# Kernel optimization log

Measured on AMD Instinct MI355X. Metric: run time of the kernel, lower is better.

The kernel has to match this reference:

```python
import jax, jax.numpy as jnp
import numpy as np

N_HEAD = 12
LN_EPS = 1e-5


def _layernorm(x, g, b):
    m = jnp.mean(x, axis=-1, keepdims=True)
    v = jnp.mean(jnp.square(x - m), axis=-1, keepdims=True)
    return (x - m) * jax.lax.rsqrt(v + LN_EPS) * g + b


def _block(x, p):
    # p holds single-layer params. x: [B, S, D]
    B, S, D = x.shape
    Dh = D // N_HEAD
    h = _layernorm(x, p['ln1_g'], p['ln1_b'])
    q = (h @ p['wq'] + p['bq']).reshape(B, S, N_HEAD, Dh)
    k = (h @ p['wk'] + p['bk']).reshape(B, S, N_HEAD, Dh)
    v = (h @ p['wv'] + p['bv']).reshape(B, S, N_HEAD, Dh)
    scores = jnp.einsum('bqhd,bkhd->bhqk', q, k) / np.sqrt(Dh).astype(x.dtype)
    causal = jnp.tril(jnp.ones((S, S), dtype=bool))  # valid_nums = arange(1..S)
    scores = jnp.where(causal, scores, -jnp.inf)
    attn = jax.nn.softmax(scores, axis=-1)  # dropout is identity in eval
    o = jnp.einsum('bhqk,bkhd->bqhd', attn, v).reshape(B, S, D)
    x = x + o @ p['wo'] + p['bo']
    h2 = _layernorm(x, p['ln2_g'], p['ln2_b'])
    ff = jax.nn.gelu(h2 @ p['w1'] + p['b1'], approximate=False) @ p['w2'] + p['b2']
    return x + ff


def _gpt_forward(idx, wte, wpe, layer_params, lnf_g, lnf_b, lm_w):
    S = idx.shape[1]
    x = wte[idx] + wpe[None, :S, :]  # embd dropout is identity in eval
    x = jax.lax.scan(lambda c, p: (_block(c, p), None), x, layer_params)[0]
    x = _layernorm(x, lnf_g, lnf_b)
    return x @ lm_w  # logits [B, S, V]


def setup_inputs() -> dict:
    B, S, D, V, L, F = 4, 1024, 768, 50257, 12, 3072
    key = jax.random.key(0)
    ks = iter(jax.random.split(key, 24))
    std = 0.02
    std_proj = 0.02 / np.sqrt(2 * L)  # special init for w_o / FFN.linear2

    def w(shape, s=std):
        return jax.random.normal(next(ks), shape, jnp.float32) * s

    return dict(
        idx=jax.random.randint(next(ks), (B, S), 0, V),
        wte=w((V, D)), wpe=w((S, D)),
        ln1_g=jnp.ones((L, D)), ln1_b=jnp.zeros((L, D)),
        wq=w((L, D, D)), bq=jnp.zeros((L, D)),
        wk=w((L, D, D)), bk=jnp.zeros((L, D)),
        wv=w((L, D, D)), bv=jnp.zeros((L, D)),
        wo=w((L, D, D), std_proj), bo=jnp.zeros((L, D)),
        ln2_g=jnp.ones((L, D)), ln2_b=jnp.zeros((L, D)),
        w1=w((L, D, F)), b1=jnp.zeros((L, F)),
        w2=w((L, F, D), std_proj), b2=jnp.zeros((L, D)),
        lnf_g=jnp.ones((D,)), lnf_b=jnp.zeros((D,)),
        lm_w=w((D, V)),
    )


def reference(idx, wte, wpe, ln1_g, ln1_b, wq, bq, wk, bk, wv, bv, wo, bo,
              ln2_g, ln2_b, w1, b1, w2, b2, lnf_g, lnf_b, lm_w):
    layer_params = dict(ln1_g=ln1_g, ln1_b=ln1_b, wq=wq, bq=bq, wk=wk, bk=bk,
                        wv=wv, bv=bv, wo=wo, bo=bo, ln2_g=ln2_g, ln2_b=ln2_b,
                        w1=w1, b1=b1, w2=w2, b2=b2)
    return _gpt_forward(idx, wte, wpe, layer_params, lnf_g, lnf_b, lm_w)
```

## Files before the change

kernel.cpp:

```cpp
#include <hip/hip_runtime.h>
#include <hip/hip_bf16.h>

typedef __attribute__((ext_vector_type(8))) short short8;
typedef __attribute__((ext_vector_type(4))) short short4v;
typedef __attribute__((ext_vector_type(4))) float floatx4;

#define GLD16(g, l) __builtin_amdgcn_global_load_lds( \
    (__attribute__((address_space(1))) void*)(g),      \
    (__attribute__((address_space(3))) void*)(l), 16, 0, 0)

#define MFMA_BF16(a, b, c) __builtin_amdgcn_mfma_f32_16x16x32_bf16((a), (b), (c), 0, 0, 0)

__device__ __forceinline__ short f2bf(float f) {
  union { __hip_bfloat16 h; short s; } u;
  u.h = __float2bfloat16(f);
  return u.s;
}

template <int N>
__device__ __forceinline__ void wait_vm() {
  if constexpr (N == 0) asm volatile("s_waitcnt vmcnt(0)" ::: "memory");
  else if constexpr (N == 4) asm volatile("s_waitcnt vmcnt(4)" ::: "memory");
  else if constexpr (N == 6) asm volatile("s_waitcnt vmcnt(6)" ::: "memory");
}
__device__ __forceinline__ void cfence() { asm volatile("" ::: "memory"); }

__global__ __launch_bounds__(256)
void transpose_convert(const float* __restrict__ in, short* __restrict__ out,
                       const int K, const int N, const size_t inStride,
                       const size_t outStride) {
  in += blockIdx.z * inStride;
  out += blockIdx.z * outStride;
  __shared__ float tile[32][33];
  const int n0 = blockIdx.x * 32;
  const int k0 = blockIdx.y * 32;
  const int tx = threadIdx.x;
  const int ty = threadIdx.y;
#pragma unroll
  for (int i = 0; i < 4; ++i) {
    const int kk = ty + i * 8;
    const int nn = n0 + tx;
    tile[kk][tx] = (nn < N) ? in[(size_t)(k0 + kk) * N + nn] : 0.f;
  }
  __syncthreads();
#pragma unroll
  for (int i = 0; i < 4; ++i) {
    const int nn = ty + i * 8;
    out[(size_t)(n0 + nn) * K + k0 + tx] = f2bf(tile[tx][nn]);
  }
}

__global__ __launch_bounds__(256)
void embed_kernel(const int* __restrict__ idx, const float* __restrict__ wte,
                  const float* __restrict__ wpe, float* __restrict__ x) {
  const int row = blockIdx.x;
  const int tok = idx[row];
  const int s = row & 1023;
  const float* wt = wte + (size_t)tok * 768;
  const float* wp = wpe + (size_t)s * 768;
  float* xr = x + (size_t)row * 768;
  for (int c = threadIdx.x; c < 768; c += 256) xr[c] = wt[c] + wp[c];
}

__global__ __launch_bounds__(256)
void ln_kernel(const float* __restrict__ x, const float* __restrict__ g,
               const float* __restrict__ b, short* __restrict__ out) {
  const int wv = threadIdx.x >> 6, lane = threadIdx.x & 63;
  const int row = blockIdx.x * 4 + wv;
  const float* xr = x + (size_t)row * 768 + lane * 12;
  const float4 a0 = *(const float4*)(xr);
  const float4 a1 = *(const float4*)(xr + 4);
  const float4 a2 = *(const float4*)(xr + 8);
  float v[12] = {a0.x, a0.y, a0.z, a0.w, a1.x, a1.y, a1.z, a1.w,
                 a2.x, a2.y, a2.z, a2.w};
  float s = 0.f;
#pragma unroll
  for (int i = 0; i < 12; ++i) s += v[i];
#pragma unroll
  for (int m = 1; m < 64; m <<= 1) s += __shfl_xor(s, m);
  const float mean = s * (1.0f / 768.0f);
  float q = 0.f;
#pragma unroll
  for (int i = 0; i < 12; ++i) {
    v[i] -= mean;
    q += v[i] * v[i];
  }
#pragma unroll
  for (int m = 1; m < 64; m <<= 1) q += __shfl_xor(q, m);
  const float inv = rsqrtf(q * (1.0f / 768.0f) + 1e-5f);

  const float* gp = g + lane * 12;
  const float* bp = b + lane * 12;
  const float4 g0 = *(const float4*)(gp);
  const float4 g1 = *(const float4*)(gp + 4);
  const float4 g2 = *(const float4*)(gp + 8);
  const float4 b0 = *(const float4*)(bp);
  const float4 b1 = *(const float4*)(bp + 4);
  const float4 b2 = *(const float4*)(bp + 8);
  const float gg[12] = {g0.x, g0.y, g0.z, g0.w, g1.x, g1.y, g1.z, g1.w,
                        g2.x, g2.y, g2.z, g2.w};
  const float bb[12] = {b0.x, b0.y, b0.z, b0.w, b1.x, b1.y, b1.z, b1.w,
                        b2.x, b2.y, b2.z, b2.w};
  short r[12];
#pragma unroll
  for (int i = 0; i < 12; ++i) r[i] = f2bf(v[i] * inv * gg[i] + bb[i]);
  short* orow = out + (size_t)row * 768 + lane * 12;
#pragma unroll
  for (int i = 0; i < 3; ++i)
    *(short4v*)(orow + i * 4) = short4v{r[i * 4], r[i * 4 + 1], r[i * 4 + 2],
                                        r[i * 4 + 3]};
}

enum { EPI_QKV = 0, EPI_RESID = 1, EPI_GELU = 2 };

template <int BM, int BN, int EPI>
__global__ __launch_bounds__(256)
void gemm_kernel(const short* __restrict__ A, const short* __restrict__ Bt,
                 const int K,
                 const float* __restrict__ bias0, const float* __restrict__ bias1,
                 const float* __restrict__ bias2, float* __restrict__ fout,
                 short* __restrict__ bout0, short* __restrict__ bout1,
                 short* __restrict__ bout2) {
  constexpr int MF = BM / 32;
  constexpr int NF = BN / 32;
  constexpr int NL = MF + NF;
  __shared__ short sA[2][BM * 64];
  __shared__ short sB[2][BN * 64];
  const int tid = threadIdx.x;
  const int wv = tid >> 6;
  const int lane = tid & 63;
  const int lrow = lane & 15;
  const int lk8 = lane >> 4;
  const int m0 = blockIdx.x * BM;
  const int n0 = blockIdx.y * BN;
  const int wm = (wv >> 1) * (BM / 2);
  const int wn = (wv & 1) * (BN / 2);
  constexpr int MW = BM / 2 / 16;
  constexpr int NW = BN / 2 / 16;

  floatx4 acc[MW][NW];
#pragma unroll
  for (int m = 0; m < MW; ++m)
#pragma unroll
    for (int n = 0; n < NW; ++n) acc[m][n] = {0.f, 0.f, 0.f, 0.f};

  const short* pA[MF];
  const short* pB[NF];
#pragma unroll
  for (int i = 0; i < MF; ++i) {
    const int p = i * 256 + tid;
    const int rr = p >> 3, up = p & 7;
    pA[i] = A + (size_t)(m0 + rr) * K + ((up ^ (rr & 7)) << 3);
  }
#pragma unroll
  for (int i = 0; i < NF; ++i) {
    const int p = i * 256 + tid;
    const int rr = p >> 3, up = p & 7;
    pB[i] = Bt + (size_t)(n0 + rr) * K + ((up ^ (rr & 7)) << 3);
  }

  auto stage = [&](int buf) {
#pragma unroll
    for (int i = 0; i < MF; ++i) {
      GLD16(pA[i], sA[buf] + (i * 256 + wv * 64) * 8);
      pA[i] += 64;
    }
#pragma unroll
    for (int i = 0; i < NF; ++i) {
      GLD16(pB[i], sB[buf] + (i * 256 + wv * 64) * 8);
      pB[i] += 64;
    }
  };

  auto compute = [&](const short* pa, const short* pb) {
    const int xr = lrow & 7;
    short8 af[MW][2], bv[NW][2];
#pragma unroll
    for (int m = 0; m < MW; ++m) {
      const int row = (wm + m * 16 + lrow) * 64;
      af[m][0] = *(const short8*)(pa + row + ((lk8 ^ xr) << 3));
      af[m][1] = *(const short8*)(pa + row + (((4 + lk8) ^ xr) << 3));
    }
#pragma unroll
    for (int n = 0; n < NW; ++n) {
      const int row = (wn + n * 16 + lrow) * 64;
      bv[n][0] = *(const short8*)(pb + row + ((lk8 ^ xr) << 3));
      bv[n][1] = *(const short8*)(pb + row + (((4 + lk8) ^ xr) << 3));
    }
#pragma unroll
    for (int m = 0; m < MW; ++m)
#pragma unroll
      for (int n = 0; n < NW; ++n) {
        acc[m][n] = MFMA_BF16(af[m][0], bv[n][0], acc[m][n]);
        acc[m][n] = MFMA_BF16(af[m][1], bv[n][1], acc[m][n]);
      }
  };

  const int nk = K >> 6;
  stage(0);
  int cur = 0;
  for (int kt = 0; kt < nk; ++kt) {
    if (kt + 1 < nk) {
      stage(cur ^ 1);
      wait_vm<NL>();
    } else {
      wait_vm<0>();
    }
    __builtin_amdgcn_s_barrier();
    cfence();
    __builtin_amdgcn_s_setprio(1);
    compute(sA[cur], sB[cur]);
    __builtin_amdgcn_s_setprio(0);
    cfence();
    __builtin_amdgcn_s_barrier();
    cur ^= 1;
  }

#pragma unroll
  for (int m = 0; m < MW; ++m) {
#pragma unroll
    for (int n = 0; n < NW; ++n) {
#pragma unroll
      for (int r = 0; r < 4; ++r) {
        const float v = acc[m][n][r];
        const int gm = m0 + wm + m * 16 + lk8 * 4 + r;
        const int gn = n0 + wn + n * 16 + lrow;
        if (EPI == EPI_QKV) {
          const int sec = (gn >= 1536) ? 2 : (gn >= 768 ? 1 : 0);
          const int nn = gn - sec * 768;
          const int hh = nn >> 6, dh = nn & 63;
          const int bb = gm >> 10, srow = gm & 1023;
          if (sec == 0) {
            bout0[(((size_t)(bb * 12 + hh) * 1024 + srow) << 6) + dh] =
                f2bf((v + bias0[nn]) * 0.18033688f);
          } else if (sec == 1) {
            bout1[(((size_t)(bb * 12 + hh) * 1024 + srow) << 6) + dh] =
                f2bf(v + bias1[nn]);
          } else {
            bout2[(((size_t)(bb * 12 + hh) * 64 + dh) << 10) + srow] =
                f2bf(v + bias2[nn]);
          }
        } else if (EPI == EPI_RESID) {
          float* xp = fout + (size_t)gm * 768 + gn;
          *xp = *xp + v + bias0[gn];
        } else {
          const float tt = v + bias0[gn];
          const float gl = 0.5f * tt * (1.f + erff(tt * 0.70710678118654752f));
          bout0[(size_t)gm * 3072 + gn] = f2bf(gl);
        }
      }
    }
  }
}

__global__ __launch_bounds__(512, 2)
void gemm_lm_kernel(const short* __restrict__ A, const short* __restrict__ Bt,
                    float* __restrict__ fout) {
  __shared__ short sA[2][256 * 64];
  __shared__ short sB[2][128 * 64];
  const int K = 768;
  const int tid = threadIdx.x;
  const int wv = tid >> 6;
  const int lane = tid & 63;
  const int lrow = lane & 15;
  const int lk8 = lane >> 4;
  const int m0 = blockIdx.x * 256;
  const int n0 = blockIdx.y * 128;
  const int wm = (wv >> 1) * 64;
  const int wn = (wv & 1) * 64;

  floatx4 acc[4][4];
#pragma unroll
  for (int m = 0; m < 4; ++m)
#pragma unroll
    for (int n = 0; n < 4; ++n) acc[m][n] = {0.f, 0.f, 0.f, 0.f};

  const short* Ab = A + (size_t)m0 * K;
  const short* Bb = Bt + (size_t)n0 * K;

  const short* pA[4];
  const short* pB[2];
#pragma unroll
  for (int i = 0; i < 4; ++i) {
    const int p = i * 512 + tid;
    const int rr = p >> 3, up = p & 7;
    pA[i] = Ab + (size_t)rr * K + ((up ^ (rr & 7)) << 3);
  }
#pragma unroll
  for (int i = 0; i < 2; ++i) {
    const int p = i * 512 + tid;
    const int rr = p >> 3, up = p & 7;
    pB[i] = Bb + (size_t)rr * K + ((up ^ (rr & 7)) << 3);
  }

  auto stage = [&](int buf) {
#pragma unroll
    for (int i = 0; i < 4; ++i) {
      GLD16(pA[i], sA[buf] + (i * 512 + wv * 64) * 8);
      pA[i] += 64;
    }
#pragma unroll
    for (int i = 0; i < 2; ++i) {
      GLD16(pB[i], sB[buf] + (i * 512 + wv * 64) * 8);
      pB[i] += 64;
    }
  };

  const int arow = (wm + lrow) * 64;
  const int xr = (lrow & 7);

  stage(0);
  int cur = 0;
  for (int kt = 0; kt < 12; ++kt) {
    if (kt + 1 < 12) {
      stage(cur ^ 1);
      wait_vm<6>();
    } else {
      wait_vm<0>();
    }
    __builtin_amdgcn_s_barrier();
    cfence();

    const short* pa = sA[cur];
    const short* pb = sB[cur];
    short8 bvv[4][2];
#pragma unroll
    for (int n = 0; n < 4; ++n) {
      const int brow = (wn + n * 16 + lrow) * 64;
      bvv[n][0] = *(const short8*)(pb + brow + ((lk8 ^ xr) << 3));
      bvv[n][1] = *(const short8*)(pb + brow + (((4 + lk8) ^ xr) << 3));
    }
    __builtin_amdgcn_s_setprio(1);
#pragma unroll
    for (int m = 0; m < 4; ++m) {
      const short8 a0 = *(const short8*)(pa + arow + m * 1024 + ((lk8 ^ xr) << 3));
      const short8 a1 =
          *(const short8*)(pa + arow + m * 1024 + (((4 + lk8) ^ xr) << 3));
#pragma unroll
      for (int n = 0; n < 4; ++n) {
        acc[m][n] = MFMA_BF16(a0, bvv[n][0], acc[m][n]);
        acc[m][n] = MFMA_BF16(a1, bvv[n][1], acc[m][n]);
      }
    }
    __builtin_amdgcn_s_setprio(0);
    cfence();
    __builtin_amdgcn_s_barrier();
    cur ^= 1;
  }

#pragma unroll
  for (int m = 0; m < 4; ++m)
#pragma unroll
    for (int n = 0; n < 4; ++n)
#pragma unroll
      for (int r = 0; r < 4; ++r) {
        const int gm = m0 + wm + m * 16 + lk8 * 4 + r;
        const int gn = n0 + wn + n * 16 + lrow;
        if (gn < 50257) fout[(size_t)gm * 50257 + gn] = acc[m][n][r];
      }
}

__global__ __launch_bounds__(256)
void attn_kernel(const short* __restrict__ q, const short* __restrict__ k,
                 const short* __restrict__ vt, short* __restrict__ o) {
  __shared__ short sK[2][64 * 64];
  __shared__ short sV[2][64 * 64];
  const int bh = blockIdx.x;
  const int qi = 15 - blockIdx.y;
  const int tid = threadIdx.x;
  const int wv = tid >> 6, lane = tid & 63;
  const int lrow = lane & 15, lk8 = lane >> 4;
  const int q0 = qi * 64;
  const int qrow = q0 + wv * 16 + lrow;

  const short* qg = q + ((size_t)(bh * 1024 + qrow)) * 64 + lk8 * 8;
  const short8 qf0 = *(const short8*)qg;
  const short8 qf1 = *(const short8*)(qg + 32);

  const int e0 = tid * 8, e1 = (256 + tid) * 8;
  const int sr0 = e0 >> 6, sc0 = e0 & 63;
  const int sr1 = e1 >> 6, sc1 = e1 & 63;
  const int su0 = ((sc0 >> 3) ^ (sr0 & 7)) << 3;
  const int su1 = ((sc1 >> 3) ^ (sr1 & 7)) << 3;
  const short* kb = k + (size_t)bh * 1024 * 64;
  const short* vb = vt + (size_t)bh * 64 * 1024;

  short8 kreg0, kreg1, vreg0, vreg1;
  auto load_tile = [&](int k0) {
    kreg0 = *(const short8*)(kb + (size_t)(k0 + sr0) * 64 + sc0);
    kreg1 = *(const short8*)(kb + (size_t)(k0 + sr1) * 64 + sc1);
    vreg0 = *(const short8*)(vb + (size_t)sr0 * 1024 + k0 + sc0);
    vreg1 = *(const short8*)(vb + (size_t)sr1 * 1024 + k0 + sc1);
  };
  auto write_tile = [&](short* dK, short* dV) {
    *(short8*)(dK + sr0 * 64 + su0) = kreg0;
    *(short8*)(dK + sr1 * 64 + su1) = kreg1;
    *(short8*)(dV + sr0 * 64 + su0) = vreg0;
    *(short8*)(dV + sr1 * 64 + su1) = vreg1;
  };

  float m_run = -1e30f, lsum = 0.f;
  floatx4 accO[4];
#pragma unroll
  for (int n = 0; n < 4; ++n) accO[n] = {0.f, 0.f, 0.f, 0.f};

  load_tile(0);
  write_tile(sK[0], sV[0]);
  __syncthreads();

  int cur = 0;
  for (int t = 0; t <= qi; ++t) {
    const int k0 = t * 64;
    if (t < qi) load_tile(k0 + 64);

    floatx4 accS[4];
#pragma unroll
    for (int n = 0; n < 4; ++n) accS[n] = {0.f, 0.f, 0.f, 0.f};
    const int rKb = ((lrow >> 2) << 3) + (lrow & 3);
    const short* pK = sK[cur];
    const short* pV = sV[cur];
#pragma unroll
    for (int ks = 0; ks < 2; ++ks) {
      const short8 qf = ks ? qf1 : qf0;
#pragma unroll
      for (int n = 0; n < 4; ++n) {
        const int rK = ((n >> 1) << 5) + ((n & 1) << 2) + rKb;
        const short8 kf =
            *(const short8*)(pK + rK * 64 + (((ks * 4 + lk8) ^ (rK & 7)) << 3));
        accS[n] = MFMA_BF16(kf, qf, accS[n]);
      }
    }

    float sv[4][4];
    float mx = -1e30f;
#pragma unroll
    for (int n = 0; n < 4; ++n)
#pragma unroll
      for (int r = 0; r < 4; ++r) {
        const int key = k0 + ((n >> 1) << 5) + (lk8 << 3) + ((n & 1) << 2) + r;
        float s = accS[n][r];
        s = (key > qrow) ? -1e30f : s;
        sv[n][r] = s;
        mx = fmaxf(mx, s);
      }
    mx = fmaxf(mx, __shfl_xor(mx, 16));
    mx = fmaxf(mx, __shfl_xor(mx, 32));

    const bool skip = __all(mx <= m_run + 8.0f);
    float sf = 1.f;
    if (!skip) {
      const float mnew = fmaxf(m_run, mx);
      sf = exp2f(m_run - mnew);
      m_run = mnew;
    }

    float rs = 0.f;
    unsigned int w[4][2];
#pragma unroll
    for (int n = 0; n < 4; ++n)
#pragma unroll
      for (int rp = 0; rp < 2; ++rp) {
        const float ea = exp2f(sv[n][2 * rp] - m_run);
        const float eb = exp2f(sv[n][2 * rp + 1] - m_run);
        rs += ea + eb;
        w[n][rp] = (unsigned int)(unsigned short)f2bf(ea) |
                   ((unsigned int)(unsigned short)f2bf(eb) << 16);
      }

    if (skip) {
      lsum += rs;
    } else {
      lsum = lsum * sf + rs;
      float sfq[4];
#pragma unroll
      for (int r = 0; r < 4; ++r)
        sfq[r] = __shfl(sf, (lane & 48) | (lk8 * 4 + r));
#pragma unroll
      for (int n = 0; n < 4; ++n)
#pragma unroll
        for (int r = 0; r < 4; ++r) accO[n][r] *= sfq[r];
    }

    union { short8 s; unsigned int u[4]; } paf0, paf1;
#pragma unroll
    for (int tt = 0; tt < 4; ++tt) {
      paf0.u[tt] = w[tt >> 1][tt & 1];
      paf1.u[tt] = w[2 + (tt >> 1)][tt & 1];
    }

#pragma unroll
    for (int n = 0; n < 4; ++n) {
      const int dh = n * 16 + lrow;
      const short8 vf0 = *(const short8*)(pV + dh * 64 + ((lk8 ^ (dh & 7)) << 3));
      const short8 vf1 =
          *(const short8*)(pV + dh * 64 + (((4 + lk8) ^ (dh & 7)) << 3));
      accO[n] = MFMA_BF16(paf0.s, vf0, accO[n]);
      accO[n] = MFMA_BF16(paf1.s, vf1, accO[n]);
    }

    if (t < qi) write_tile(sK[cur ^ 1], sV[cur ^ 1]);
    __syncthreads();
    cur ^= 1;
  }

  float ls = lsum;
  ls += __shfl_xor(ls, 16);
  ls += __shfl_xor(ls, 32);
  const float invown = 1.f / ls;
  float invq[4];
#pragma unroll
  for (int r = 0; r < 4; ++r)
    invq[r] = __shfl(invown, (lane & 48) | (lk8 * 4 + r));

  const int bb = bh / 12, hh = bh % 12;
#pragma unroll
  for (int n = 0; n < 4; ++n)
#pragma unroll
    for (int r = 0; r < 4; ++r) {
      const int row = q0 + wv * 16 + lk8 * 4 + r;
      const float ov = accO[n][r] * invq[r];
      o[((size_t)(bb * 1024 + row)) * 768 + hh * 64 + n * 16 + lrow] = f2bf(ov);
    }
}

extern "C" void kernel_launch(void* const* d_in, const int* in_sizes, int n_in,
                              void* d_out, int out_size, void* d_ws, size_t ws_size,
                              hipStream_t stream) {
  const int* idx = (const int*)d_in[0];
  const float* wte = (const float*)d_in[1];
  const float* wpe = (const float*)d_in[2];
  const float* ln1_g = (const float*)d_in[3];
  const float* ln1_b = (const float*)d_in[4];
  const float* wq = (const float*)d_in[5];
  const float* bq = (const float*)d_in[6];
  const float* wk = (const float*)d_in[7];
  const float* bk = (const float*)d_in[8];
  const float* wv = (const float*)d_in[9];
  const float* bv = (const float*)d_in[10];
  const float* wo = (const float*)d_in[11];
  const float* bo = (const float*)d_in[12];
  const float* ln2_g = (const float*)d_in[13];
  const float* ln2_b = (const float*)d_in[14];
  const float* w1 = (const float*)d_in[15];
  const float* b1 = (const float*)d_in[16];
  const float* w2 = (const float*)d_in[17];
  const float* b2 = (const float*)d_in[18];
  const float* lnf_g = (const float*)d_in[19];
  const float* lnf_b = (const float*)d_in[20];
  const float* lm_w = (const float*)d_in[21];
  float* out = (float*)d_out;

  char* base = (char*)d_ws;
  size_t off = 0;
  auto alloc = [&](size_t bytes) {
    char* r = base + off;
    off = (off + bytes + 255) & ~(size_t)255;
    return r;
  };
  short* lmT = (short*)alloc((size_t)50304 * 768 * 2);
  float* x = (float*)alloc((size_t)4096 * 768 * 4);
  short* h = (short*)alloc((size_t)4096 * 768 * 2);
  short* qb = (short*)alloc((size_t)4096 * 768 * 2);
  short* kb = (short*)alloc((size_t)4096 * 768 * 2);
  short* vtb = (short*)alloc((size_t)4096 * 768 * 2);
  short* ob = (short*)alloc((size_t)4096 * 768 * 2);
  short* ff = (short*)alloc((size_t)4096 * 3072 * 2);

  const size_t LW = 7077888;
  const size_t dd = (size_t)768 * 768;
  const bool big = (off + (size_t)12 * LW * 2 + 256 <= ws_size);
  short* wAll = nullptr;
  short *wqkvT = nullptr, *woT = nullptr, *w1T = nullptr, *w2T = nullptr;
  if (big) {
    wAll = (short*)alloc((size_t)12 * LW * 2);
  } else {
    wqkvT = (short*)alloc((size_t)2304 * 768 * 2);
    woT = (short*)alloc((size_t)768 * 768 * 2);
    w1T = (short*)alloc((size_t)3072 * 768 * 2);
    w2T = (short*)alloc((size_t)768 * 3072 * 2);
    if (off > ws_size) return;
  }

  const dim3 tb(32, 8);
  transpose_convert<<<dim3(1572, 24, 1), tb, 0, stream>>>(lm_w, lmT, 768, 50257, 0, 0);
  if (big) {
    transpose_convert<<<dim3(24, 24, 12), tb, 0, stream>>>(wq, wAll + 0, 768, 768, dd, LW);
    transpose_convert<<<dim3(24, 24, 12), tb, 0, stream>>>(wk, wAll + 589824, 768, 768, dd, LW);
    transpose_convert<<<dim3(24, 24, 12), tb, 0, stream>>>(wv, wAll + 1179648, 768, 768, dd, LW);
    transpose_convert<<<dim3(24, 24, 12), tb, 0, stream>>>(wo, wAll + 1769472, 768, 768, dd, LW);
    transpose_convert<<<dim3(96, 24, 12), tb, 0, stream>>>(w1, wAll + 2359296, 768, 3072,
                                                           (size_t)768 * 3072, LW);
    transpose_convert<<<dim3(24, 96, 12), tb, 0, stream>>>(w2, wAll + 4718592, 3072, 768,
                                                           (size_t)3072 * 768, LW);
  }
  embed_kernel<<<4096, 256, 0, stream>>>(idx, wte, wpe, x);

  for (int l = 0; l < 12; ++l) {
    const short *pQKV, *pWO, *pW1, *pW2;
    if (big) {
      short* wl = wAll + (size_t)l * LW;
      pQKV = wl;
      pWO = wl + 1769472;
      pW1 = wl + 2359296;
      pW2 = wl + 4718592;
    } else {
      transpose_convert<<<dim3(24, 24, 1), tb, 0, stream>>>(wq + l * dd, wqkvT, 768, 768, 0, 0);
      transpose_convert<<<dim3(24, 24, 1), tb, 0, stream>>>(wk + l * dd, wqkvT + dd, 768, 768, 0, 0);
      transpose_convert<<<dim3(24, 24, 1), tb, 0, stream>>>(wv + l * dd, wqkvT + 2 * dd, 768, 768, 0, 0);
      transpose_convert<<<dim3(24, 24, 1), tb, 0, stream>>>(wo + l * dd, woT, 768, 768, 0, 0);
      transpose_convert<<<dim3(96, 24, 1), tb, 0, stream>>>(w1 + (size_t)l * 768 * 3072, w1T, 768, 3072, 0, 0);
      transpose_convert<<<dim3(24, 96, 1), tb, 0, stream>>>(w2 + (size_t)l * 3072 * 768, w2T, 3072, 768, 0, 0);
      pQKV = wqkvT; pWO = woT; pW1 = w1T; pW2 = w2T;
    }

    ln_kernel<<<1024, 256, 0, stream>>>(x, ln1_g + l * 768, ln1_b + l * 768, h);
    gemm_kernel<128, 64, EPI_QKV><<<dim3(32, 36), 256, 0, stream>>>(
        h, pQKV, 768, bq + l * 768, bk + l * 768, bv + l * 768, nullptr, qb, kb, vtb);
    attn_kernel<<<dim3(48, 16), 256, 0, stream>>>(qb, kb, vtb, ob);
    gemm_kernel<64, 64, EPI_RESID><<<dim3(64, 12), 256, 0, stream>>>(
        ob, pWO, 768, bo + l * 768, nullptr, nullptr, x, nullptr, nullptr, nullptr);
    ln_kernel<<<1024, 256, 0, stream>>>(x, ln2_g + l * 768, ln2_b + l * 768, h);
    gemm_kernel<128, 64, EPI_GELU><<<dim3(32, 48), 256, 0, stream>>>(
        h, pW1, 768, b1 + l * 3072, nullptr, nullptr, nullptr, ff, nullptr, nullptr);
    gemm_kernel<64, 64, EPI_RESID><<<dim3(64, 12), 256, 0, stream>>>(
        ff, pW2, 3072, b2 + l * 768, nullptr, nullptr, x, nullptr, nullptr, nullptr);
  }

  ln_kernel<<<1024, 256, 0, stream>>>(x, lnf_g, lnf_b, h);
  gemm_lm_kernel<<<dim3(16, 393), 512, 0, stream>>>(h, lmT, out);
}
```

Baseline: 2.942 ms.

## Enlarge LM-head GEMM tile to 256x256 with staged half-tile prefetch

The LM-head GEMM tile grows from 256x128 to 256x256, with 8 waves each computing 128x64. Global-to-LDS prefetch of the next k-slice is split into four quarter-stages interleaved with the MFMA phases, and the padded vocab size is raised so the grid divides evenly. The aim is more reuse of the A operand and less redundant traffic on the dominant final projection. In exchange it doubles the accumulator registers, drops the two-blocks-per-CU occupancy hint, and uses more LDS. The generic GEMM loop is also simplified to plain __syncthreads with no explicit vmcnt waits and no priority hints, which may lose overlap between loads and compute.

```diff
diff --git a/kernel.cpp b/kernel.cpp
--- a/kernel.cpp
+++ b/kernel.cpp
@@ -20,8 +20,7 @@
 template <int N>
 __device__ __forceinline__ void wait_vm() {
   if constexpr (N == 0) asm volatile("s_waitcnt vmcnt(0)" ::: "memory");
-  else if constexpr (N == 4) asm volatile("s_waitcnt vmcnt(4)" ::: "memory");
-  else if constexpr (N == 6) asm volatile("s_waitcnt vmcnt(6)" ::: "memory");
+  else if constexpr (N == 2) asm volatile("s_waitcnt vmcnt(2)" ::: "memory");
 }
 __device__ __forceinline__ void cfence() { asm volatile("" ::: "memory"); }
 
@@ -123,7 +122,6 @@
                  short* __restrict__ bout2) {
   constexpr int MF = BM / 32;
   constexpr int NF = BN / 32;
-  constexpr int NL = MF + NF;
   __shared__ short sA[2][BM * 64];
   __shared__ short sB[2][BN * 64];
   const int tid = threadIdx.x;
@@ -198,21 +196,12 @@
 
   const int nk = K >> 6;
   stage(0);
+  __syncthreads();
   int cur = 0;
   for (int kt = 0; kt < nk; ++kt) {
-    if (kt + 1 < nk) {
-      stage(cur ^ 1);
-      wait_vm<NL>();
-    } else {
-      wait_vm<0>();
-    }
-    __builtin_amdgcn_s_barrier();
-    cfence();
-    __builtin_amdgcn_s_setprio(1);
+    if (kt + 1 < nk) stage(cur ^ 1);
     compute(sA[cur], sB[cur]);
-    __builtin_amdgcn_s_setprio(0);
-    cfence();
-    __builtin_amdgcn_s_barrier();
+    __syncthreads();
     cur ^= 1;
   }
 
@@ -253,11 +242,11 @@
   }
 }
 
-__global__ __launch_bounds__(512, 2)
+__global__ __launch_bounds__(512)
 void gemm_lm_kernel(const short* __restrict__ A, const short* __restrict__ Bt,
                     float* __restrict__ fout) {
   __shared__ short sA[2][256 * 64];
-  __shared__ short sB[2][128 * 64];
+  __shared__ short sB[2][256 * 64];
   const int K = 768;
   const int tid = threadIdx.x;
   const int wv = tid >> 6;
@@ -265,91 +254,89 @@
   const int lrow = lane & 15;
   const int lk8 = lane >> 4;
   const int m0 = blockIdx.x * 256;
-  const int n0 = blockIdx.y * 128;
-  const int wm = (wv >> 1) * 64;
-  const int wn = (wv & 1) * 64;
-
-  floatx4 acc[4][4];
-#pragma unroll
-  for (int m = 0; m < 4; ++m)
+  const int n0 = blockIdx.y * 256;
+  const int wm = (wv >> 2) * 128;
+  const int wn = (wv & 3) * 64;
+  const int xr = lrow & 7;
+
+  floatx4 acc[8][4];
+#pragma unroll
+  for (int m = 0; m < 8; ++m)
 #pragma unroll
     for (int n = 0; n < 4; ++n) acc[m][n] = {0.f, 0.f, 0.f, 0.f};
 
-  const short* Ab = A + (size_t)m0 * K;
-  const short* Bb = Bt + (size_t)n0 * K;
-
-  const short* pA[4];
-  const short* pB[2];
-#pragma unroll
-  for (int i = 0; i < 4; ++i) {
-    const int p = i * 512 + tid;
-    const int rr = p >> 3, up = p & 7;
-    pA[i] = Ab + (size_t)rr * K + ((up ^ (rr & 7)) << 3);
-  }
-#pragma unroll
-  for (int i = 0; i < 2; ++i) {
-    const int p = i * 512 + tid;
-    const int rr = p >> 3, up = p & 7;
-    pB[i] = Bb + (size_t)rr * K + ((up ^ (rr & 7)) << 3);
-  }
-
-  auto stage = [&](int buf) {
-#pragma unroll
-    for (int i = 0; i < 4; ++i) {
-      GLD16(pA[i], sA[buf] + (i * 512 + wv * 64) * 8);
-      pA[i] += 64;
-    }
+  const short* pH[4][2];
+#pragma unroll
+  for (int h = 0; h < 4; ++h)
 #pragma unroll
     for (int i = 0; i < 2; ++i) {
-      GLD16(pB[i], sB[buf] + (i * 512 + wv * 64) * 8);
-      pB[i] += 64;
+      const int slot = i * 512 + tid;
+      const int rr = (slot >> 3) + (h & 1) * 128;
+      const int up = slot & 7;
+      const short* gb = (h < 2) ? (A + (size_t)(m0 + rr) * K)
+                                : (Bt + (size_t)(n0 + rr) * K);
+      pH[h][i] = gb + ((up ^ (rr & 7)) << 3);
+    }
+
+  auto stage_half = [&](int buf, int h) {
+    short* dst = ((h < 2) ? sA[buf] : sB[buf]) + (h & 1) * 8192;
+#pragma unroll
+    for (int i = 0; i < 2; ++i) {
+      GLD16(pH[h][i], dst + (i * 512 + wv * 64) * 8);
+      pH[h][i] += 64;
     }
   };
 
-  const int arow = (wm + lrow) * 64;
-  const int xr = (lrow & 7);
-
-  stage(0);
+#pragma unroll
+  for (int h = 0; h < 4; ++h) stage_half(0, h);
+
   int cur = 0;
   for (int kt = 0; kt < 12; ++kt) {
-    if (kt + 1 < 12) {
-      stage(cur ^ 1);
-      wait_vm<6>();
-    } else {
-      wait_vm<0>();
-    }
+    const short* pa = sA[cur];
+    const short* pb = sB[cur];
+#pragma unroll
+    for (int p = 0; p < 4; ++p) {
+      const int mh = p >> 1, nh = p & 1;
+      if (kt + 1 < 12) stage_half(cur ^ 1, p);
+      if (p == 0) {
+        if (kt + 1 < 12) wait_vm<2>();
+        else wait_vm<0>();
+        __builtin_amdgcn_s_barrier();
+        cfence();
+      }
+      short8 af[4][2], bv[2][2];
+#pragma unroll
+      for (int mi = 0; mi < 4; ++mi) {
+        const int row = (wm + mh * 64 + mi * 16 + lrow) * 64;
+        af[mi][0] = *(const short8*)(pa + row + ((lk8 ^ xr) << 3));
+        af[mi][1] = *(const short8*)(pa + row + (((4 + lk8) ^ xr) << 3));
+      }
+#pragma unroll
+      for (int ni = 0; ni < 2; ++ni) {
+        const int row = (wn + nh * 32 + ni * 16 + lrow) * 64;
+        bv[ni][0] = *(const short8*)(pb + row + ((lk8 ^ xr) << 3));
+        bv[ni][1] = *(const short8*)(pb + row + (((4 + lk8) ^ xr) << 3));
+      }
+      __builtin_amdgcn_s_setprio(1);
+#pragma unroll
+      for (int mi = 0; mi < 4; ++mi)
+#pragma unroll
+        for (int ni = 0; ni < 2; ++ni) {
+          acc[mh * 4 + mi][nh * 2 + ni] =
+              MFMA_BF16(af[mi][0], bv[ni][0], acc[mh * 4 + mi][nh * 2 + ni]);
+          acc[mh * 4 + mi][nh * 2 + ni] =
+              MFMA_BF16(af[mi][1], bv[ni][1], acc[mh * 4 + mi][nh * 2 + ni]);
+        }
+      __builtin_amdgcn_s_setprio(0);
+    }
+    cfence();
     __builtin_amdgcn_s_barrier();
     cfence();
-
-    const short* pa = sA[cur];
-    const short* pb = sB[cur];
-    short8 bvv[4][2];
-#pragma unroll
-    for (int n = 0; n < 4; ++n) {
-      const int brow = (wn + n * 16 + lrow) * 64;
-      bvv[n][0] = *(const short8*)(pb + brow + ((lk8 ^ xr) << 3));
-      bvv[n][1] = *(const short8*)(pb + brow + (((4 + lk8) ^ xr) << 3));
-    }
-    __builtin_amdgcn_s_setprio(1);
-#pragma unroll
-    for (int m = 0; m < 4; ++m) {
-      const short8 a0 = *(const short8*)(pa + arow + m * 1024 + ((lk8 ^ xr) << 3));
-      const short8 a1 =
-          *(const short8*)(pa + arow + m * 1024 + (((4 + lk8) ^ xr) << 3));
-#pragma unroll
-      for (int n = 0; n < 4; ++n) {
-        acc[m][n] = MFMA_BF16(a0, bvv[n][0], acc[m][n]);
-        acc[m][n] = MFMA_BF16(a1, bvv[n][1], acc[m][n]);
-      }
-    }
-    __builtin_amdgcn_s_setprio(0);
-    cfence();
-    __builtin_amdgcn_s_barrier();
     cur ^= 1;
   }
 
 #pragma unroll
-  for (int m = 0; m < 4; ++m)
+  for (int m = 0; m < 8; ++m)
 #pragma unroll
     for (int n = 0; n < 4; ++n)
 #pragma unroll
@@ -557,7 +544,7 @@
     off = (off + bytes + 255) & ~(size_t)255;
     return r;
   };
-  short* lmT = (short*)alloc((size_t)50304 * 768 * 2);
+  short* lmT = (short*)alloc((size_t)50432 * 768 * 2);
   float* x = (float*)alloc((size_t)4096 * 768 * 4);
   short* h = (short*)alloc((size_t)4096 * 768 * 2);
   short* qb = (short*)alloc((size_t)4096 * 768 * 2);
@@ -582,7 +569,7 @@
   }
 
   const dim3 tb(32, 8);
-  transpose_convert<<<dim3(1572, 24, 1), tb, 0, stream>>>(lm_w, lmT, 768, 50257, 0, 0);
+  transpose_convert<<<dim3(1576, 24, 1), tb, 0, stream>>>(lm_w, lmT, 768, 50257, 0, 0);
   if (big) {
     transpose_convert<<<dim3(24, 24, 12), tb, 0, stream>>>(wq, wAll + 0, 768, 768, dd, LW);
     transpose_convert<<<dim3(24, 24, 12), tb, 0, stream>>>(wk, wAll + 589824, 768, 768, dd, LW);
@@ -627,5 +614,5 @@
   }
 
   ln_kernel<<<1024, 256, 0, stream>>>(x, lnf_g, lnf_b, h);
-  gemm_lm_kernel<<<dim3(16, 393), 512, 0, stream>>>(h, lmT, out);
-}
+  gemm_lm_kernel<<<dim3(16, 197), 512, 0, stream>>>(h, lmT, out);
+}
```

Measured after the change: 2.987 ms. Within noise of the previous version (+1.6%).
